# Kernel optimization log

Hardware: AMD Instinct MI355X
Metric: run time of the kernel (lower is better)

## Reference

```python
import jax, jax.numpy as jnp
import numpy as np

DIM = 1024
HEADS = 16
HEAD_DIM = DIM // HEADS
MLP_HID = 4 * DIM
EPS = 1e-5


def layer_norm(x, g, b):
    mu = jnp.mean(x, axis=-1, keepdims=True)
    var = jnp.mean(jnp.square(x - mu), axis=-1, keepdims=True)
    return (x - mu) * jax.lax.rsqrt(var + EPS) * g + b


def setup_inputs() -> dict:
    key = jax.random.key(0)
    ks = jax.random.split(key, 8)
    s_in = 1.0 / np.sqrt(DIM)
    s_hid = 1.0 / np.sqrt(MLP_HID)
    return {
        "x": jax.random.normal(ks[0], (4, 2048, DIM), dtype=jnp.float32),
        "qkv_w": jax.random.uniform(ks[1], (3 * DIM, DIM), jnp.float32, -s_in, s_in),
        "proj_w": jax.random.uniform(ks[2], (DIM, DIM), jnp.float32, -s_in, s_in),
        "proj_b": jnp.zeros((DIM,), jnp.float32),
        "ln1_g": jnp.ones((DIM,), jnp.float32),
        "ln1_b": jnp.zeros((DIM,), jnp.float32),
        "w1": jax.random.uniform(ks[3], (MLP_HID, DIM), jnp.float32, -s_in, s_in),
        "b1": jnp.zeros((MLP_HID,), jnp.float32),
        "prelu_a": jnp.asarray(0.25, jnp.float32),
        "w2": jax.random.uniform(ks[4], (DIM, MLP_HID), jnp.float32, -s_hid, s_hid),
        "b2": jnp.zeros((DIM,), jnp.float32),
        "ln2_g": jnp.ones((DIM,), jnp.float32),
        "ln2_b": jnp.zeros((DIM,), jnp.float32),
    }


def reference(x, qkv_w, proj_w, proj_b, ln1_g, ln1_b, w1, b1, prelu_a, w2, b2, ln2_g, ln2_b):
    B, N, C = x.shape
    scale = HEAD_DIM ** (-0.5)

    # Multi-head self-attention (full NxN scores, softmax over keys)
    qkv = (x @ qkv_w.T).reshape(B, N, 3, HEADS, HEAD_DIM)
    qkv = jnp.transpose(qkv, (2, 0, 3, 1, 4))  # [3, B, H, N, hd]
    q, k, v = qkv[0] * scale, qkv[1], qkv[2]
    attn = jax.nn.softmax(jnp.einsum("bhnd,bhmd->bhnm", q, k), axis=-1)
    o = jnp.einsum("bhnm,bhmd->bhnd", attn, v)
    o = jnp.transpose(o, (0, 2, 1, 3)).reshape(B, N, C)
    o = o @ proj_w.T + proj_b

    # Post-norm residual 1
    x = layer_norm(x + o, ln1_g, ln1_b)

    # MLP: Linear -> (Dropout=identity in eval) -> PReLU -> Linear
    h = x @ w1.T + b1
    h = jnp.where(h >= 0, h, prelu_a * h)
    h = h @ w2.T + b2

    # Post-norm residual 2
    return layer_norm(x + h, ln2_g, ln2_b)
```

## Files before the change

### kernel.cpp

```cpp
#include <hip/hip_runtime.h>


typedef __attribute__((ext_vector_type(8))) short short8;
typedef __attribute__((ext_vector_type(4))) short short4v;
typedef __attribute__((ext_vector_type(4))) float floatx4;
typedef __attribute__((ext_vector_type(4))) int int4v;

__device__ __forceinline__ float bf2f(unsigned short u) {
    return __uint_as_float(((unsigned int)u) << 16);
}
__device__ __forceinline__ unsigned short f2bf(float f) {
    unsigned int u = __float_as_uint(f);
    u += 0x7FFFu + ((u >> 16) & 1u);
    return (unsigned short)(u >> 16);
}
__device__ __forceinline__ int pack2bf(float a, float b) {
    return (int)f2bf(a) | ((int)f2bf(b) << 16);
}
__device__ __forceinline__ unsigned int cvt_pk_bf16(float lo, float hi) {
    unsigned int r;
    asm("v_cvt_pk_bf16_f32 %0, %1, %2" : "=v"(r) : "v"(lo), "v"(hi));
    return r;
}

#define Q_PRESCALE 0.18033688011112043f

#if __has_builtin(__builtin_amdgcn_exp2f)
__device__ __forceinline__ float fast_exp2(float x) { return __builtin_amdgcn_exp2f(x); }
#else
__device__ __forceinline__ float fast_exp2(float x) { return __expf(x * 0.6931471805599453f); }
#endif

#if __has_builtin(__builtin_amdgcn_permlane32_swap) && __has_builtin(__builtin_amdgcn_permlane16_swap)
#define HAVE_PERMLANE 1
#else
#define HAVE_PERMLANE 0
#endif

__device__ __forceinline__ void async16(const unsigned short* g, unsigned short* l) {
    __builtin_amdgcn_global_load_lds(
        (const __attribute__((address_space(1))) unsigned int*)g,
        (__attribute__((address_space(3))) unsigned int*)l, 16, 0, 0);
}

__global__ __launch_bounds__(256)
void cvt_f2b(const float* __restrict__ in, unsigned short* __restrict__ out) {
    const int i = (blockIdx.x * 256 + threadIdx.x) * 4;
    float4 v = *(const float4*)&in[i];
    short4v o;
    o[0] = (short)f2bf(v.x); o[1] = (short)f2bf(v.y);
    o[2] = (short)f2bf(v.z); o[3] = (short)f2bf(v.w);
    *(short4v*)&out[i] = o;
}

__global__ __launch_bounds__(512, 2)
void gemm256(const unsigned short* __restrict__ A,
             const unsigned short* __restrict__ W,
             const float* __restrict__ bias,
             const float* __restrict__ prelu,
             unsigned short* __restrict__ C,
             int N, int K, int qcols, int NNT) {
    __shared__ alignas(16) unsigned short lA[2][256 * 64];
    __shared__ alignas(16) unsigned short lB[2][256 * 64];

    const int nwg = gridDim.x;
    const int orig = blockIdx.x;
    const int q8 = nwg >> 3, r8 = nwg & 7, xx = orig & 7, rest = orig >> 3;
    const int wgid = (xx < r8 ? xx * (q8 + 1) : r8 * (q8 + 1) + (xx - r8) * q8) + rest;
    const int mt = wgid / NNT, nt = wgid % NNT;
    const int m0 = mt * 256, n0 = nt * 256;

    const int tid  = threadIdx.x;
    const int lane = tid & 63;
    const int wave = tid >> 6;
    const int lr = lane & 15, lq = lane >> 4;
    const int wrow = (wave >> 2) * 64;
    const int wcol = (wave & 3) * 32;
    const int srow = lane >> 3;
    const int scol = ((lane & 7) * 8) ^ ((lane & 32) ? 16 : 0);
    const int kxo  = (lq * 8) ^ ((lr & 4) ? 16 : 0);

    const int NT = K >> 6;

    floatx4 acc[2][2][4][2] = {};

    auto stA = [&](int d, int tt, int h) {
        #pragma unroll
        for (int it = 0; it < 2; ++it) {
            const int rb = h * 128 + (wave * 2 + it) * 8;
            async16(&A[(size_t)(m0 + rb + srow) * K + tt * 64 + scol], &lA[d][rb * 64]);
        }
    };
    auto stB = [&](int d, int tt, int h) {
        #pragma unroll
        for (int it = 0; it < 2; ++it) {
            const int rb = h * 128 + (wave * 2 + it) * 8;
            async16(&W[(size_t)(n0 + rb + srow) * K + tt * 64 + scol], &lB[d][rb * 64]);
        }
    };

    stA(0, 0, 0); stB(0, 0, 0); stB(0, 0, 1); stA(0, 0, 1);
    stA(1, 1, 0); stB(1, 1, 0); stB(1, 1, 1);
    asm volatile("s_waitcnt vmcnt(6)" ::: "memory");
    __builtin_amdgcn_s_barrier();
    asm volatile("" ::: "memory");

    short8 af[4][2], b0[2][2], b1[2][2];

    for (int t = 0; t < NT; ++t) {
        const int d = t & 1, e = d ^ 1;

        #pragma unroll
        for (int i = 0; i < 4; ++i)
            #pragma unroll
            for (int s = 0; s < 2; ++s)
                af[i][s] = *(const short8*)&lA[d][(wrow + i * 16 + lr) * 64 + s * 32 + kxo];
        #pragma unroll
        for (int j = 0; j < 2; ++j)
            #pragma unroll
            for (int s = 0; s < 2; ++s)
                b0[j][s] = *(const short8*)&lB[d][(wcol + j * 16 + lr) * 64 + s * 32 + kxo];
        if (t + 1 < NT) stA(e, t + 1, 1);
        __builtin_amdgcn_s_barrier();
        asm volatile("s_waitcnt lgkmcnt(0)" ::: "memory");
        __builtin_amdgcn_s_setprio(1);
        #pragma unroll
        for (int s = 0; s < 2; ++s)
            #pragma unroll
            for (int i = 0; i < 4; ++i)
                #pragma unroll
                for (int j = 0; j < 2; ++j)
                    acc[0][0][i][j] = __builtin_amdgcn_mfma_f32_16x16x32_bf16(
                        af[i][s], b0[j][s], acc[0][0][i][j], 0, 0, 0);
        __builtin_amdgcn_s_setprio(0);
        __builtin_amdgcn_s_barrier();
        asm volatile("" ::: "memory");

        #pragma unroll
        for (int j = 0; j < 2; ++j)
            #pragma unroll
            for (int s = 0; s < 2; ++s)
                b1[j][s] = *(const short8*)&lB[d][(128 + wcol + j * 16 + lr) * 64 + s * 32 + kxo];
        if (t + 2 < NT) stA(d, t + 2, 0);
        __builtin_amdgcn_s_barrier();
        asm volatile("s_waitcnt lgkmcnt(0)" ::: "memory");
        __builtin_amdgcn_s_setprio(1);
        #pragma unroll
        for (int s = 0; s < 2; ++s)
            #pragma unroll
            for (int i = 0; i < 4; ++i)
                #pragma unroll
                for (int j = 0; j < 2; ++j)
                    acc[0][1][i][j] = __builtin_amdgcn_mfma_f32_16x16x32_bf16(
                        af[i][s], b1[j][s], acc[0][1][i][j], 0, 0, 0);
        __builtin_amdgcn_s_setprio(0);
        __builtin_amdgcn_s_barrier();
        asm volatile("" ::: "memory");

        #pragma unroll
        for (int i = 0; i < 4; ++i)
            #pragma unroll
            for (int s = 0; s < 2; ++s)
                af[i][s] = *(const short8*)&lA[d][(128 + wrow + i * 16 + lr) * 64 + s * 32 + kxo];
        if (t + 2 < NT) stB(d, t + 2, 0);
        __builtin_amdgcn_s_barrier();
        asm volatile("s_waitcnt lgkmcnt(0)" ::: "memory");
        __builtin_amdgcn_s_setprio(1);
        #pragma unroll
        for (int s = 0; s < 2; ++s)
            #pragma unroll
            for (int i = 0; i < 4; ++i)
                #pragma unroll
                for (int j = 0; j < 2; ++j)
                    acc[1][1][i][j] = __builtin_amdgcn_mfma_f32_16x16x32_bf16(
                        af[i][s], b1[j][s], acc[1][1][i][j], 0, 0, 0);
        __builtin_amdgcn_s_setprio(0);
        __builtin_amdgcn_s_barrier();
        asm volatile("" ::: "memory");

        if (t + 2 < NT) stB(d, t + 2, 1);
        __builtin_amdgcn_s_barrier();
        asm volatile("" ::: "memory");
        __builtin_amdgcn_s_setprio(1);
        #pragma unroll
        for (int s = 0; s < 2; ++s)
            #pragma unroll
            for (int i = 0; i < 4; ++i)
                #pragma unroll
                for (int j = 0; j < 2; ++j)
                    acc[1][0][i][j] = __builtin_amdgcn_mfma_f32_16x16x32_bf16(
                        af[i][s], b0[j][s], acc[1][0][i][j], 0, 0, 0);
        __builtin_amdgcn_s_setprio(0);
        if (t + 2 < NT) {
            asm volatile("s_waitcnt vmcnt(6)" ::: "memory");
        } else {
            asm volatile("s_waitcnt vmcnt(0)" ::: "memory");
        }
        __builtin_amdgcn_s_barrier();
        asm volatile("" ::: "memory");
    }

    const bool hasb = (bias != nullptr);
    const bool hasp = (prelu != nullptr);
    const float slope = hasp ? prelu[0] : 0.f;
    #pragma unroll
    for (int mh = 0; mh < 2; ++mh)
        #pragma unroll
        for (int nh = 0; nh < 2; ++nh)
            #pragma unroll
            for (int j = 0; j < 2; ++j) {
                const int gc = n0 + nh * 128 + wcol + j * 16 + lr;
                const float bv = hasb ? bias[gc] : 0.f;
                const float cs = (gc < qcols) ? Q_PRESCALE : 1.f;
                #pragma unroll
                for (int i = 0; i < 4; ++i) {
                    const int gr = m0 + mh * 128 + wrow + i * 16 + lq * 4;
                    #pragma unroll
                    for (int r = 0; r < 4; ++r) {
                        float v = acc[mh][nh][i][j][r] + bv;
                        if (hasp && v < 0.f) v *= slope;
                        C[(size_t)(gr + r) * N + gc] = f2bf(v * cs);
                    }
                }
            }
}

__global__ __launch_bounds__(256)
void transpose_v(const unsigned short* __restrict__ qkv,
                 unsigned short* __restrict__ vt) {
    const int kt = blockIdx.x;
    const int bh = blockIdx.y;
    const int b = bh >> 4, h = bh & 15;
    __shared__ unsigned short tile[64 * 65];
    for (int t = threadIdx.x; t < 512; t += 256) {
        const int key = t >> 3, c8 = (t & 7) << 3;
        short8 v8 = *(const short8*)&qkv[((size_t)(b * 2048 + kt * 64 + key)) * 3072 +
                                         2048 + h * 64 + c8];
        #pragma unroll
        for (int e = 0; e < 8; ++e)
            tile[key * 65 + c8 + e] = (unsigned short)v8[e];
    }
    __syncthreads();
    for (int t = threadIdx.x; t < 512; t += 256) {
        const int d = t >> 3, k8 = (t & 7) << 3;
        short8 o;
        #pragma unroll
        for (int e = 0; e < 8; ++e)
            o[e] = (short)tile[(k8 + e) * 65 + d];
        *(short8*)&vt[((size_t)bh * 64 + d) * 2048 + kt * 64 + k8] = o;
    }
}

__global__ __launch_bounds__(256, 2)
void attn_kernel(const unsigned short* __restrict__ qkv,
                 const unsigned short* __restrict__ vt,
                 unsigned short* __restrict__ o_attn) {
    const int id = blockIdx.x;
    const int qg = id >> 6;
    const int bh = id & 63;
    const int b = bh >> 4, h = bh & 15;
    const int tid  = threadIdx.x;
    const int lane = tid & 63;
    const int wave = tid >> 6;
    const int lr = lane & 15;
    const int lq = lane >> 4;
    const int q0 = (qg * 4 + wave) * 64;
    const size_t row0 = (size_t)(b * 2048) * 3072;

    __shared__ alignas(16) unsigned short lK[2][64 * 64];
    __shared__ alignas(16) unsigned short lV[2][64 * 64];

    short8 qf[4][2];
    #pragma unroll
    for (int j = 0; j < 4; ++j)
        #pragma unroll
        for (int s = 0; s < 2; ++s)
            qf[j][s] = *(const short8*)&qkv[row0 + (size_t)(q0 + j * 16 + lr) * 3072 +
                                            h * 64 + s * 32 + lq * 8];

    floatx4 oacc[4][4] = {};
    float l_i[4] = {0.f, 0.f, 0.f, 0.f};

    const int srow = lane >> 3;
    const int scol = (((lane & 7) ^ srow)) << 3;
    const int kx = lr & 7;

    auto stage = [&](int bi, int kc) {
        #pragma unroll
        for (int it2 = 0; it2 < 2; ++it2) {
            const int it = wave * 2 + it2;
            const int row = it * 8 + srow;
            async16(&qkv[row0 + (size_t)(kc + row) * 3072 + 1024 + h * 64 + scol],
                    &lK[bi][it * 512 + lane * 8]);
            async16(&vt[((size_t)bh * 64 + row) * 2048 + kc + scol],
                    &lV[bi][it * 512 + lane * 8]);
        }
    };

    asm volatile("s_waitcnt vmcnt(0)" ::: "memory");
    stage(0, 0);

    #pragma unroll 1
    for (int c = 0; c < 32; ++c) {
        const int cur = c & 1;
        if (c + 1 < 32) {
            stage(cur ^ 1, (c + 1) * 64);
            asm volatile("s_waitcnt vmcnt(4)" ::: "memory");
        } else {
            asm volatile("s_waitcnt vmcnt(0)" ::: "memory");
        }
        __builtin_amdgcn_s_barrier();
        asm volatile("" ::: "memory");

        floatx4 sacc[4][4] = {};
        #pragma unroll
        for (int s = 0; s < 2; ++s) {
            short8 kf[4];
            #pragma unroll
            for (int i = 0; i < 4; ++i) {
                const int r = i * 16 + lr;
                kf[i] = *(const short8*)&lK[cur][r * 64 + (((s * 4 + lq) ^ kx) << 3)];
            }
            #pragma unroll
            for (int i = 0; i < 4; ++i)
                #pragma unroll
                for (int j = 0; j < 4; ++j)
                    sacc[i][j] = __builtin_amdgcn_mfma_f32_16x16x32_bf16(
                        kf[i], qf[j][s], sacc[i][j], 0, 0, 0);
        }

        unsigned int pkd[4][4][2];
        #pragma unroll
        for (int i = 0; i < 4; ++i)
            #pragma unroll
            for (int j = 0; j < 4; ++j) {
                const float e0 = fast_exp2(sacc[i][j][0]);
                const float e1 = fast_exp2(sacc[i][j][1]);
                const float e2 = fast_exp2(sacc[i][j][2]);
                const float e3 = fast_exp2(sacc[i][j][3]);
                l_i[j] += (e0 + e1) + (e2 + e3);
                pkd[i][j][0] = cvt_pk_bf16(e0, e1);
                pkd[i][j][1] = cvt_pk_bf16(e2, e3);
            }

        #pragma unroll
        for (int s = 0; s < 2; ++s) {
            short8 vf[4];
            #pragma unroll
            for (int i = 0; i < 4; ++i) {
                const int r = i * 16 + lr;
                vf[i] = *(const short8*)&lV[cur][r * 64 + (((s * 4 + lq) ^ kx) << 3)];
            }
            short8 bq[4];
            #pragma unroll
            for (int j = 0; j < 4; ++j) {
                int4v iv;
#if HAVE_PERMLANE
                auto p0 = __builtin_amdgcn_permlane32_swap(
                    pkd[2 * s][j][0], pkd[2 * s + 1][j][0], false, false);
                auto w0 = __builtin_amdgcn_permlane16_swap(p0[0], p0[1], false, false);
                auto p1 = __builtin_amdgcn_permlane32_swap(
                    pkd[2 * s][j][1], pkd[2 * s + 1][j][1], false, false);
                auto w1 = __builtin_amdgcn_permlane16_swap(p1[0], p1[1], false, false);
                iv[0] = (int)w0[0]; iv[1] = (int)w1[0];
                iv[2] = (int)w0[1]; iv[3] = (int)w1[1];
#else
                const int src0 = lr + ((lq & 1) * 2) * 16;
                const int src1 = src0 + 16;
                const bool hi = (lq >> 1) != 0;
                int a0 = __shfl((int)pkd[2 * s][j][0], src0, 64);
                int c0 = __shfl((int)pkd[2 * s + 1][j][0], src0, 64);
                int a1 = __shfl((int)pkd[2 * s][j][1], src0, 64);
                int c1 = __shfl((int)pkd[2 * s + 1][j][1], src0, 64);
                int a2 = __shfl((int)pkd[2 * s][j][0], src1, 64);
                int c2 = __shfl((int)pkd[2 * s + 1][j][0], src1, 64);
                int a3 = __shfl((int)pkd[2 * s][j][1], src1, 64);
                int c3 = __shfl((int)pkd[2 * s + 1][j][1], src1, 64);
                iv[0] = hi ? c0 : a0;
                iv[1] = hi ? c1 : a1;
                iv[2] = hi ? c2 : a2;
                iv[3] = hi ? c3 : a3;
#endif
                bq[j] = __builtin_bit_cast(short8, iv);
            }
            #pragma unroll
            for (int j = 0; j < 4; ++j)
                #pragma unroll
                for (int i = 0; i < 4; ++i)
                    oacc[i][j] = __builtin_amdgcn_mfma_f32_16x16x32_bf16(
                        vf[i], bq[j], oacc[i][j], 0, 0, 0);
        }

        asm volatile("s_waitcnt lgkmcnt(0)" ::: "memory");
        __builtin_amdgcn_s_barrier();
        asm volatile("" ::: "memory");
    }

    #pragma unroll
    for (int j = 0; j < 4; ++j) {
        l_i[j] += __shfl_xor(l_i[j], 16, 64);
        l_i[j] += __shfl_xor(l_i[j], 32, 64);
        const float rl = 1.f / l_i[j];
        const int q = q0 + j * 16 + lr;
        #pragma unroll
        for (int i = 0; i < 4; ++i) {
            int2 pk;
            pk.x = pack2bf(oacc[i][j][0] * rl, oacc[i][j][1] * rl);
            pk.y = pack2bf(oacc[i][j][2] * rl, oacc[i][j][3] * rl);
            *(int2*)&o_attn[((size_t)(b * 2048 + q)) * 1024 + h * 64 + i * 16 + lq * 4] = pk;
        }
    }
}

__global__ __launch_bounds__(256)
void ln_f32_bf16(const float* __restrict__ x,
                 const unsigned short* __restrict__ res,
                 const float* __restrict__ g,
                 const float* __restrict__ bta,
                 unsigned short* __restrict__ out) {
    const int row = blockIdx.x;
    const int t = threadIdx.x;
    const size_t base = (size_t)row * 1024;

    float4 xv = *(const float4*)&x[base + t * 4];
    short4v rv = *(const short4v*)&res[base + t * 4];
    float v[4] = { xv.x + bf2f((unsigned short)rv[0]),
                   xv.y + bf2f((unsigned short)rv[1]),
                   xv.z + bf2f((unsigned short)rv[2]),
                   xv.w + bf2f((unsigned short)rv[3]) };
    float s = 0.f, s2 = 0.f;
    #pragma unroll
    for (int k = 0; k < 4; ++k) { s += v[k]; s2 += v[k] * v[k]; }
    #pragma unroll
    for (int off = 32; off > 0; off >>= 1) {
        s  += __shfl_xor(s, off, 64);
        s2 += __shfl_xor(s2, off, 64);
    }
    __shared__ float red[8];
    const int wave = t >> 6;
    if ((t & 63) == 0) { red[wave] = s; red[4 + wave] = s2; }
    __syncthreads();
    s  = red[0] + red[1] + red[2] + red[3];
    s2 = red[4] + red[5] + red[6] + red[7];
    const float mean = s * (1.f / 1024.f);
    const float var  = fmaxf(s2 * (1.f / 1024.f) - mean * mean, 0.f);
    const float inv  = rsqrtf(var + 1e-5f);

    short4v ov;
    #pragma unroll
    for (int k = 0; k < 4; ++k) {
        int c = t * 4 + k;
        ov[k] = (short)f2bf((v[k] - mean) * inv * g[c] + bta[c]);
    }
    *(short4v*)&out[base + t * 4] = ov;
}

__global__ __launch_bounds__(256)
void ln_bf16_f32(const unsigned short* __restrict__ x,
                 const unsigned short* __restrict__ res,
                 const float* __restrict__ g,
                 const float* __restrict__ bta,
                 float* __restrict__ out) {
    const int row = blockIdx.x;
    const int t = threadIdx.x;
    const size_t base = (size_t)row * 1024;

    short4v xv = *(const short4v*)&x[base + t * 4];
    short4v rv = *(const short4v*)&res[base + t * 4];
    float v[4];
    float s = 0.f, s2 = 0.f;
    #pragma unroll
    for (int k = 0; k < 4; ++k) {
        v[k] = bf2f((unsigned short)xv[k]) + bf2f((unsigned short)rv[k]);
        s += v[k];
        s2 += v[k] * v[k];
    }
    #pragma unroll
    for (int off = 32; off > 0; off >>= 1) {
        s  += __shfl_xor(s, off, 64);
        s2 += __shfl_xor(s2, off, 64);
    }
    __shared__ float red[8];
    const int wave = t >> 6;
    if ((t & 63) == 0) { red[wave] = s; red[4 + wave] = s2; }
    __syncthreads();
    s  = red[0] + red[1] + red[2] + red[3];
    s2 = red[4] + red[5] + red[6] + red[7];
    const float mean = s * (1.f / 1024.f);
    const float var  = fmaxf(s2 * (1.f / 1024.f) - mean * mean, 0.f);
    const float inv  = rsqrtf(var + 1e-5f);

    float4 ov;
    ov.x = (v[0] - mean) * inv * g[t * 4 + 0] + bta[t * 4 + 0];
    ov.y = (v[1] - mean) * inv * g[t * 4 + 1] + bta[t * 4 + 1];
    ov.z = (v[2] - mean) * inv * g[t * 4 + 2] + bta[t * 4 + 2];
    ov.w = (v[3] - mean) * inv * g[t * 4 + 3] + bta[t * 4 + 3];
    *(float4*)&out[base + t * 4] = ov;
}

extern "C" void kernel_launch(void* const* d_in, const int* in_sizes, int n_in,
                              void* d_out, int out_size, void* d_ws, size_t ws_size,
                              hipStream_t stream) {
    const float* x      = (const float*)d_in[0];
    const float* qkv_w  = (const float*)d_in[1];
    const float* proj_w = (const float*)d_in[2];
    const float* proj_b = (const float*)d_in[3];
    const float* ln1_g  = (const float*)d_in[4];
    const float* ln1_b  = (const float*)d_in[5];
    const float* w1     = (const float*)d_in[6];
    const float* b1     = (const float*)d_in[7];
    const float* prelu  = (const float*)d_in[8];
    const float* w2     = (const float*)d_in[9];
    const float* b2     = (const float*)d_in[10];
    const float* ln2_g  = (const float*)d_in[11];
    const float* ln2_b  = (const float*)d_in[12];
    float* out = (float*)d_out;

    char* ws = (char*)d_ws;
    const size_t MB = 1024 * 1024;
    unsigned short* wqkvb  = (unsigned short*)(ws);
    unsigned short* wprojb = (unsigned short*)(ws + 6 * MB);
    unsigned short* w1b    = (unsigned short*)(ws + 8 * MB);
    unsigned short* w2b    = (unsigned short*)(ws + 16 * MB);
    unsigned short* xb     = (unsigned short*)(ws + 24 * MB);
    unsigned short* vtb    = (unsigned short*)(ws + 24 * MB);
    unsigned short* qkvb   = (unsigned short*)(ws + 40 * MB);
    unsigned short* oat    = (unsigned short*)(ws + 88 * MB);
    unsigned short* pout   = (unsigned short*)(ws + 24 * MB);
    unsigned short* x1b    = (unsigned short*)(ws + 40 * MB);
    unsigned short* h1     = (unsigned short*)(ws + 56 * MB);
    unsigned short* h2     = (unsigned short*)(ws + 24 * MB);

    cvt_f2b<<<8192, 256, 0, stream>>>(x,      xb);
    cvt_f2b<<<3072, 256, 0, stream>>>(qkv_w,  wqkvb);
    cvt_f2b<<<1024, 256, 0, stream>>>(proj_w, wprojb);
    cvt_f2b<<<4096, 256, 0, stream>>>(w1,     w1b);
    cvt_f2b<<<4096, 256, 0, stream>>>(w2,     w2b);

    gemm256<<<dim3(32 * 12), 512, 0, stream>>>(xb, wqkvb, nullptr, nullptr,
                                               qkvb, 3072, 1024, 1024, 12);
    transpose_v<<<dim3(32, 64), 256, 0, stream>>>(qkvb, vtb);
    attn_kernel<<<512, 256, 0, stream>>>(qkvb, vtb, oat);
    gemm256<<<dim3(32 * 4), 512, 0, stream>>>(oat, wprojb, proj_b, nullptr,
                                              pout, 1024, 1024, 0, 4);
    ln_f32_bf16<<<8192, 256, 0, stream>>>(x, pout, ln1_g, ln1_b, x1b);
    gemm256<<<dim3(32 * 16), 512, 0, stream>>>(x1b, w1b, b1, prelu,
                                               h1, 4096, 1024, 0, 16);
    gemm256<<<dim3(32 * 4), 512, 0, stream>>>(h1, w2b, b2, nullptr,
                                              h2, 1024, 4096, 0, 4);
    ln_bf16_f32<<<8192, 256, 0, stream>>>(x1b, h2, ln2_g, ln2_b, out);
}
```

Before: 567.9 us.

## Add 128x256-tile GEMM for small-N layers and switch LDS swizzle to XOR-8

Adds a gemm128 kernel with a 128-row M tile and two workgroups per CU, and uses it for the QKV, projection and second MLP GEMMs. With N=1024 the 256x256 tiles gave only 128 workgroups for 256 CUs; the smaller tile doubles the grid to fill the GPU, at the cost of less data reuse per tile. It also replaces the LDS swizzle in both GEMM kernels with a full 8-way XOR of the 16-byte column chunk by row, to cut bank conflicts on the MFMA operand reads.

```diff
diff --git a/kernel.cpp b/kernel.cpp
--- a/kernel.cpp
+++ b/kernel.cpp
@@ -77,8 +77,8 @@
     const int wrow = (wave >> 2) * 64;
     const int wcol = (wave & 3) * 32;
     const int srow = lane >> 3;
-    const int scol = ((lane & 7) * 8) ^ ((lane & 32) ? 16 : 0);
-    const int kxo  = (lq * 8) ^ ((lr & 4) ? 16 : 0);
+    const int scol = ((lane & 7) ^ srow) << 3;
+    const int kx = lr & 7;
 
     const int NT = K >> 6;
 
@@ -114,12 +114,14 @@
         for (int i = 0; i < 4; ++i)
             #pragma unroll
             for (int s = 0; s < 2; ++s)
-                af[i][s] = *(const short8*)&lA[d][(wrow + i * 16 + lr) * 64 + s * 32 + kxo];
+                af[i][s] = *(const short8*)&lA[d][(wrow + i * 16 + lr) * 64 +
+                                                 (((s * 4 + lq) ^ kx) << 3)];
         #pragma unroll
         for (int j = 0; j < 2; ++j)
             #pragma unroll
             for (int s = 0; s < 2; ++s)
-                b0[j][s] = *(const short8*)&lB[d][(wcol + j * 16 + lr) * 64 + s * 32 + kxo];
+                b0[j][s] = *(const short8*)&lB[d][(wcol + j * 16 + lr) * 64 +
+                                                 (((s * 4 + lq) ^ kx) << 3)];
         if (t + 1 < NT) stA(e, t + 1, 1);
         __builtin_amdgcn_s_barrier();
         asm volatile("s_waitcnt lgkmcnt(0)" ::: "memory");
@@ -140,7 +142,8 @@
         for (int j = 0; j < 2; ++j)
             #pragma unroll
             for (int s = 0; s < 2; ++s)
-                b1[j][s] = *(const short8*)&lB[d][(128 + wcol + j * 16 + lr) * 64 + s * 32 + kxo];
+                b1[j][s] = *(const short8*)&lB[d][(128 + wcol + j * 16 + lr) * 64 +
+                                                 (((s * 4 + lq) ^ kx) << 3)];
         if (t + 2 < NT) stA(d, t + 2, 0);
         __builtin_amdgcn_s_barrier();
         asm volatile("s_waitcnt lgkmcnt(0)" ::: "memory");
@@ -161,7 +164,8 @@
         for (int i = 0; i < 4; ++i)
             #pragma unroll
             for (int s = 0; s < 2; ++s)
-                af[i][s] = *(const short8*)&lA[d][(128 + wrow + i * 16 + lr) * 64 + s * 32 + kxo];
+                af[i][s] = *(const short8*)&lA[d][(128 + wrow + i * 16 + lr) * 64 +
+                                                 (((s * 4 + lq) ^ kx) << 3)];
         if (t + 2 < NT) stB(d, t + 2, 0);
         __builtin_amdgcn_s_barrier();
         asm volatile("s_waitcnt lgkmcnt(0)" ::: "memory");
@@ -223,6 +227,143 @@
                     }
                 }
             }
+}
+
+__global__ __launch_bounds__(512, 2)
+void gemm128(const unsigned short* __restrict__ A,
+             const unsigned short* __restrict__ W,
+             const float* __restrict__ bias,
+             const float* __restrict__ prelu,
+             unsigned short* __restrict__ C,
+             int N, int K, int qcols, int NNT) {
+    __shared__ alignas(16) unsigned short lA[2][128 * 64];
+    __shared__ alignas(16) unsigned short lB[2][256 * 64];
+
+    const int nwg = gridDim.x;
+    const int orig = blockIdx.x;
+    const int q8 = nwg >> 3, r8 = nwg & 7, xx = orig & 7, rest = orig >> 3;
+    const int wgid = (xx < r8 ? xx * (q8 + 1) : r8 * (q8 + 1) + (xx - r8) * q8) + rest;
+    const int mt = wgid / NNT, nt = wgid % NNT;
+    const int m0 = mt * 128, n0 = nt * 256;
+
+    const int tid  = threadIdx.x;
+    const int lane = tid & 63;
+    const int wave = tid >> 6;
+    const int lr = lane & 15, lq = lane >> 4;
+    const int wrow = (wave >> 2) * 64;
+    const int wcol = (wave & 3) * 32;
+    const int srow = lane >> 3;
+    const int scol = ((lane & 7) ^ srow) << 3;
+    const int kx = lr & 7;
+
+    const int NT = K >> 6;
+
+    floatx4 acc[2][4][2] = {};
+
+    auto stA = [&](int d, int tt) {
+        #pragma unroll
+        for (int it = 0; it < 2; ++it) {
+            const int rb = (wave * 2 + it) * 8;
+            async16(&A[(size_t)(m0 + rb + srow) * K + tt * 64 + scol], &lA[d][rb * 64]);
+        }
+    };
+    auto stB = [&](int d, int tt, int h) {
+        #pragma unroll
+        for (int it = 0; it < 2; ++it) {
+            const int rb = (wave * 2 + it) * 8;
+            async16(&W[(size_t)(n0 + h * 128 + rb + srow) * K + tt * 64 + scol],
+                    &lB[d][(h * 128 + rb) * 64]);
+        }
+    };
+
+    stA(0, 0); stB(0, 0, 0); stB(0, 0, 1);
+    stA(1, 1); stB(1, 1, 0);
+    asm volatile("s_waitcnt vmcnt(4)" ::: "memory");
+    __builtin_amdgcn_s_barrier();
+    asm volatile("" ::: "memory");
+
+    short8 af[4][2], b0[2][2], b1[2][2];
+
+    for (int t = 0; t < NT; ++t) {
+        const int d = t & 1, e = d ^ 1;
+
+        #pragma unroll
+        for (int i = 0; i < 4; ++i)
+            #pragma unroll
+            for (int s = 0; s < 2; ++s)
+                af[i][s] = *(const short8*)&lA[d][(wrow + i * 16 + lr) * 64 +
+                                                 (((s * 4 + lq) ^ kx) << 3)];
+        #pragma unroll
+        for (int j = 0; j < 2; ++j)
+            #pragma unroll
+            for (int s = 0; s < 2; ++s)
+                b0[j][s] = *(const short8*)&lB[d][(wcol + j * 16 + lr) * 64 +
+                                                 (((s * 4 + lq) ^ kx) << 3)];
+        if (t + 1 < NT) stB(e, t + 1, 1);
+        __builtin_amdgcn_s_barrier();
+        asm volatile("s_waitcnt lgkmcnt(0)" ::: "memory");
+        __builtin_amdgcn_s_setprio(1);
+        #pragma unroll
+        for (int s = 0; s < 2; ++s)
+            #pragma unroll
+            for (int i = 0; i < 4; ++i)
+                #pragma unroll
+                for (int j = 0; j < 2; ++j)
+                    acc[0][i][j] = __builtin_amdgcn_mfma_f32_16x16x32_bf16(
+                        af[i][s], b0[j][s], acc[0][i][j], 0, 0, 0);
+        __builtin_amdgcn_s_setprio(0);
+        __builtin_amdgcn_s_barrier();
+        asm volatile("" ::: "memory");
+
+        #pragma unroll
+        for (int j = 0; j < 2; ++j)
+            #pragma unroll
+            for (int s = 0; s < 2; ++s)
+                b1[j][s] = *(const short8*)&lB[d][(128 + wcol + j * 16 + lr) * 64 +
+                                                 (((s * 4 + lq) ^ kx) << 3)];
+        if (t + 2 < NT) { stA(d, t + 2); stB(d, t + 2, 0); }
+        __builtin_amdgcn_s_barrier();
+        asm volatile("s_waitcnt lgkmcnt(0)" ::: "memory");
+        __builtin_amdgcn_s_setprio(1);
+        #pragma unroll
+        for (int s = 0; s < 2; ++s)
+            #pragma unroll
+            for (int i = 0; i < 4; ++i)
+                #pragma unroll
+                for (int j = 0; j < 2; ++j)
+                    acc[1][i][j] = __builtin_amdgcn_mfma_f32_16x16x32_bf16(
+                        af[i][s], b1[j][s], acc[1][i][j], 0, 0, 0);
+        __builtin_amdgcn_s_setprio(0);
+        if (t + 2 < NT) {
+            asm volatile("s_waitcnt vmcnt(4)" ::: "memory");
+        } else {
+            asm volatile("s_waitcnt vmcnt(0)" ::: "memory");
+        }
+        __builtin_amdgcn_s_barrier();
+        asm volatile("" ::: "memory");
+    }
+
+    const bool hasb = (bias != nullptr);
+    const bool hasp = (prelu != nullptr);
+    const float slope = hasp ? prelu[0] : 0.f;
+    #pragma unroll
+    for (int nh = 0; nh < 2; ++nh)
+        #pragma unroll
+        for (int j = 0; j < 2; ++j) {
+            const int gc = n0 + nh * 128 + wcol + j * 16 + lr;
+            const float bv = hasb ? bias[gc] : 0.f;
+            const float cs = (gc < qcols) ? Q_PRESCALE : 1.f;
+            #pragma unroll
+            for (int i = 0; i < 4; ++i) {
+                const int gr = m0 + wrow + i * 16 + lq * 4;
+                #pragma unroll
+                for (int r = 0; r < 4; ++r) {
+                    float v = acc[nh][i][j][r] + bv;
+                    if (hasp && v < 0.f) v *= slope;
+                    C[(size_t)(gr + r) * N + gc] = f2bf(v * cs);
+                }
+            }
+        }
 }
 
 __global__ __launch_bounds__(256)
@@ -537,16 +678,16 @@
     cvt_f2b<<<4096, 256, 0, stream>>>(w1,     w1b);
     cvt_f2b<<<4096, 256, 0, stream>>>(w2,     w2b);
 
-    gemm256<<<dim3(32 * 12), 512, 0, stream>>>(xb, wqkvb, nullptr, nullptr,
+    gemm128<<<dim3(64 * 12), 512, 0, stream>>>(xb, wqkvb, nullptr, nullptr,
                                                qkvb, 3072, 1024, 1024, 12);
     transpose_v<<<dim3(32, 64), 256, 0, stream>>>(qkvb, vtb);
     attn_kernel<<<512, 256, 0, stream>>>(qkvb, vtb, oat);
-    gemm256<<<dim3(32 * 4), 512, 0, stream>>>(oat, wprojb, proj_b, nullptr,
+    gemm128<<<dim3(64 * 4), 512, 0, stream>>>(oat, wprojb, proj_b, nullptr,
                                               pout, 1024, 1024, 0, 4);
     ln_f32_bf16<<<8192, 256, 0, stream>>>(x, pout, ln1_g, ln1_b, x1b);
     gemm256<<<dim3(32 * 16), 512, 0, stream>>>(x1b, w1b, b1, prelu,
                                                h1, 4096, 1024, 0, 16);
-    gemm256<<<dim3(32 * 4), 512, 0, stream>>>(h1, w2b, b2, nullptr,
+    gemm128<<<dim3(64 * 4), 512, 0, stream>>>(h1, w2b, b2, nullptr,
                                               h2, 1024, 4096, 0, 4);
     ln_bf16_f32<<<8192, 256, 0, stream>>>(x1b, h2, ln2_g, ln2_b, out);
 }
```

Result: faster. 485.8 us (-14.5%).
